# Performance work log

Hardware: AMD Instinct MI355X
Metric: run time of the kernel (lower is better)

Reference implementation:

```python
import jax, jax.numpy as jnp
import numpy as np

C_QKV = 128
C_HID = 32
N_HEADS = 4
INF = 1e9


def setup_inputs() -> dict:
    key = jax.random.key(0)
    ks = jax.random.split(key, 8)
    B, S = 256, 256
    hc = N_HEADS * C_HID  # 128
    inp = {
        "input_qkv": jax.random.normal(ks[0], (1, B, S, C_QKV), dtype=jnp.float32),
        "mask": jnp.ones((1, B, 1, 1, S), dtype=jnp.float32),
        "bias": jax.random.normal(ks[1], (1, 1, N_HEADS, S, S), dtype=jnp.float32),
        "add_transposed_output_to": jax.random.normal(ks[2], (1, B, S, C_QKV), dtype=jnp.float32),
        # linear_qkvg: Linear(c_qkv, 4*h*c), bias=False -> weight [4*hc, c_qkv]
        "W_qkvg": jax.random.normal(ks[3], (4 * hc, C_QKV), dtype=jnp.float32) * (1.0 / np.sqrt(C_QKV)),
        # gating bias initialized to ones in the module
        "linear_g_bias": jnp.ones((hc,), dtype=jnp.float32),
        # linear_o: Linear(hc, c_qkv), init='final' (zeros in AF2, use small random for a nontrivial test)
        "W_o": jax.random.normal(ks[4], (C_QKV, hc), dtype=jnp.float32) * (1.0 / np.sqrt(hc)),
        "b_o": jax.random.normal(ks[5], (C_QKV,), dtype=jnp.float32) * 0.02,
    }
    return inp


def reference(input_qkv, mask, bias, add_transposed_output_to, W_qkvg, linear_g_bias, W_o, b_o):
    hc = N_HEADS * C_HID
    # fused QKVG projection: [1, b, s, 4*hc]
    qkvg = jnp.einsum("xbsc,fc->xbsf", input_qkv, W_qkvg)
    q, k, v, g = jnp.split(qkvg, 4, axis=-1)
    # reshape to heads: [1, b, s, h, c]
    shp = q.shape[:-1] + (N_HEADS, C_HID)
    q = q.reshape(shp)
    k = k.reshape(shp)
    v = v.reshape(shp)
    scale = 1.0 / np.sqrt(C_HID)
    # scores: [1, b, h, q, k]
    a = jnp.einsum("xbqhc,xbkhc->xbhqk", q * scale, k)
    a = a + (mask - 1.0) * INF + bias
    a = jax.nn.softmax(a, axis=-1)
    # attention output: [1, b, q, h, c] -> [1, b, s, hc]
    o = jnp.einsum("xbhqk,xbkhc->xbqhc", a, v)
    o = o.reshape(o.shape[:-2] + (hc,))
    # sigmoid gating
    o = o * jax.nn.sigmoid(g + linear_g_bias)
    # fused linear + transpose(-2,-3) + add
    proj = jnp.einsum("xbsf,of->xbso", o, W_o) + b_o  # [1, b, s, c_qkv]
    out = add_transposed_output_to + jnp.swapaxes(proj, -2, -3)  # [1, s, b, c_qkv]
    return out
```

## Files before the change

kernel.cpp:

```cpp
#include <hip/hip_runtime.h>
#include <math.h>

#define BB 256
#define SS 256
#define NH 4

typedef __attribute__((ext_vector_type(8))) short bfrag;
typedef __attribute__((ext_vector_type(4))) float ffrag;

__device__ inline unsigned short f2bf(float x) {
    unsigned u = __float_as_uint(x);
    u += 0x7FFF + ((u >> 16) & 1);
    return (unsigned short)(u >> 16);
}
__device__ inline float bf2f(unsigned short h) {
    return __uint_as_float(((unsigned)h) << 16);
}
__device__ inline unsigned pack2(float a, float b) {
    return (unsigned)f2bf(a) | ((unsigned)f2bf(b) << 16);
}
union FragU { unsigned u[4]; bfrag b; };

#define XB_OFF  0
#define WB_OFF  8388608
#define WOB_OFF 8454144
#define OG_OFF  8470528

__global__ __launch_bounds__(256) void k0_cast(
    const float* __restrict__ X, const float* __restrict__ W,
    const float* __restrict__ Wo, unsigned short* __restrict__ dst)
{
    const int gid = blockIdx.x * 256 + threadIdx.x;
    const int XN8 = 8388608 / 8, WN8 = 65536 / 8, WoN8 = 16384 / 8;
    const float* src;
    size_t soff, doff;
    if (gid < XN8)            { src = X;  soff = (size_t)gid * 8;                 doff = XB_OFF + soff; }
    else if (gid < XN8 + WN8) { src = W;  soff = (size_t)(gid - XN8) * 8;         doff = WB_OFF + soff; }
    else if (gid < XN8 + WN8 + WoN8) { src = Wo; soff = (size_t)(gid - XN8 - WN8) * 8; doff = WOB_OFF + soff; }
    else return;
    const float4 a = *(const float4*)(src + soff);
    const float4 b = *(const float4*)(src + soff + 4);
    unsigned r0 = pack2(a.x, a.y), r1 = pack2(a.z, a.w);
    unsigned r2 = pack2(b.x, b.y), r3 = pack2(b.z, b.w);
    uint4 o; o.x = r0; o.y = r1; o.z = r2; o.w = r3;
    *(uint4*)(dst + doff) = o;
}

__global__ __launch_bounds__(256, 2) void k_fused(
    const unsigned short* __restrict__ Xb,
    const unsigned short* __restrict__ Wb,
    const float* __restrict__ gbias,
    const float* __restrict__ mask,
    const float* __restrict__ bias,
    unsigned short* __restrict__ og)
{
    const int h = blockIdx.x, b = blockIdx.y;
    const int t = threadIdx.x;
    const int w = t >> 6, lane = t & 63, l15 = lane & 15, quad = lane >> 4;

    __shared__ unsigned short Qb[SS * 40];
    __shared__ unsigned short Kb[SS * 40];
    __shared__ unsigned short Vt[32 * 264];
    __shared__ unsigned short Gb[SS * 34];
    __shared__ float maskLds[SS];

    maskLds[t] = (mask[b * SS + t] - 1.0f) * 1e9f;

    const float qscale = 0.17677669529663687f;

    for (int half = 0; half < 2; ++half) {
        bfrag Wfr[4][4];
#pragma unroll
        for (int f4 = 0; f4 < 4; ++f4) {
            const int floc = (half * 4 + f4) * 16 + l15;
            const int grow = (floc >> 5) * 128 + h * 32 + (floc & 31);
#pragma unroll
            for (int cc = 0; cc < 4; ++cc)
                Wfr[f4][cc] = *(const bfrag*)(Wb + grow * 128 + cc * 32 + quad * 8);
        }
#pragma unroll
        for (int st = 0; st < 4; ++st) {
            const int s = w * 64 + st * 16 + l15;
            bfrag Xfr[4];
#pragma unroll
            for (int cc = 0; cc < 4; ++cc)
                Xfr[cc] = *(const bfrag*)(Xb + (b * SS + s) * 128 + cc * 32 + quad * 8);
#pragma unroll
            for (int f4 = 0; f4 < 4; ++f4) {
                ffrag D = {0.f, 0.f, 0.f, 0.f};
#pragma unroll
                for (int cc = 0; cc < 4; ++cc)
                    D = __builtin_amdgcn_mfma_f32_16x16x32_bf16(Xfr[cc], Wfr[f4][cc], D, 0, 0, 0);
                const int ft = half * 4 + f4;
                const int fcol = ft * 16 + l15;
                const int srow0 = w * 64 + st * 16 + quad * 4;
                if (ft < 2) {
#pragma unroll
                    for (int r = 0; r < 4; ++r)
                        Qb[(srow0 + r) * 40 + fcol] = f2bf(D[r] * qscale);
                } else if (ft < 4) {
#pragma unroll
                    for (int r = 0; r < 4; ++r)
                        Kb[(srow0 + r) * 40 + (fcol - 32)] = f2bf(D[r]);
                } else if (ft < 6) {
                    const int base = (fcol - 64) * 264 + srow0;
                    *(unsigned*)&Vt[base]     = pack2(D[0], D[1]);
                    *(unsigned*)&Vt[base + 2] = pack2(D[2], D[3]);
                } else {
                    const int c = fcol - 96;
                    const float gb = gbias[h * 32 + c];
#pragma unroll
                    for (int r = 0; r < 4; ++r) {
                        const float g = 1.0f / (1.0f + __expf(-(D[r] + gb)));
                        Gb[(srow0 + r) * 34 + c] = f2bf(g);
                    }
                }
            }
        }
    }
    __syncthreads();

    bfrag Vfr[2][8];
#pragma unroll
    for (int ch = 0; ch < 2; ++ch)
#pragma unroll
        for (int ck = 0; ck < 8; ++ck)
            Vfr[ch][ck] = *(const bfrag*)&Vt[(ch * 16 + l15) * 264 + ck * 32 + quad * 8];

    const int srcA = l15 + ((quad & 1) * 2) * 16;
    const int srcB = srcA + 16;
    const bool hi = (quad >> 1) != 0;

    for (int qq = 0; qq < 4; ++qq) {
        const int q = w * 64 + qq * 16 + l15;
        const bfrag Qfr = *(const bfrag*)&Qb[q * 40 + quad * 8];

        ffrag S[16];
#pragma unroll
        for (int kt = 0; kt < 16; ++kt) {
            const bfrag Kfr = *(const bfrag*)&Kb[(kt * 16 + l15) * 40 + quad * 8];
            const ffrag z = {0.f, 0.f, 0.f, 0.f};
            S[kt] = __builtin_amdgcn_mfma_f32_16x16x32_bf16(Kfr, Qfr, z, 0, 0, 0);
        }

        const float* brow = bias + (h * SS + q) * SS;
        float m = -1e30f;
#pragma unroll
        for (int kt = 0; kt < 16; ++kt) {
            const float4 bv = *(const float4*)(brow + kt * 16 + quad * 4);
            const float4 mv = *(const float4*)(maskLds + kt * 16 + quad * 4);
            S[kt][0] += bv.x + mv.x; S[kt][1] += bv.y + mv.y;
            S[kt][2] += bv.z + mv.z; S[kt][3] += bv.w + mv.w;
            m = fmaxf(m, fmaxf(fmaxf(S[kt][0], S[kt][1]), fmaxf(S[kt][2], S[kt][3])));
        }
        m = fmaxf(m, __shfl_xor(m, 16, 64));
        m = fmaxf(m, __shfl_xor(m, 32, 64));

        float l = 0.f;
        unsigned pk[16][2];
#pragma unroll
        for (int kt = 0; kt < 16; ++kt) {
            const float p0 = __expf(S[kt][0] - m);
            const float p1 = __expf(S[kt][1] - m);
            const float p2 = __expf(S[kt][2] - m);
            const float p3 = __expf(S[kt][3] - m);
            l += (p0 + p1) + (p2 + p3);
            pk[kt][0] = pack2(p0, p1);
            pk[kt][1] = pack2(p2, p3);
        }
        l += __shfl_xor(l, 16, 64);
        l += __shfl_xor(l, 32, 64);

        ffrag O[2];
        O[0] = (ffrag){0.f, 0.f, 0.f, 0.f};
        O[1] = (ffrag){0.f, 0.f, 0.f, 0.f};
#pragma unroll
        for (int ck = 0; ck < 8; ++ck) {
            const unsigned a0 = (unsigned)__shfl((int)pk[2 * ck][0],     srcA, 64);
            const unsigned b0 = (unsigned)__shfl((int)pk[2 * ck + 1][0], srcA, 64);
            const unsigned a1 = (unsigned)__shfl((int)pk[2 * ck][1],     srcA, 64);
            const unsigned b1 = (unsigned)__shfl((int)pk[2 * ck + 1][1], srcA, 64);
            const unsigned a2 = (unsigned)__shfl((int)pk[2 * ck][0],     srcB, 64);
            const unsigned b2 = (unsigned)__shfl((int)pk[2 * ck + 1][0], srcB, 64);
            const unsigned a3 = (unsigned)__shfl((int)pk[2 * ck][1],     srcB, 64);
            const unsigned b3 = (unsigned)__shfl((int)pk[2 * ck + 1][1], srcB, 64);
            FragU fu;
            fu.u[0] = hi ? b0 : a0;
            fu.u[1] = hi ? b1 : a1;
            fu.u[2] = hi ? b2 : a2;
            fu.u[3] = hi ? b3 : a3;
            O[0] = __builtin_amdgcn_mfma_f32_16x16x32_bf16(Vfr[0][ck], fu.b, O[0], 0, 0, 0);
            O[1] = __builtin_amdgcn_mfma_f32_16x16x32_bf16(Vfr[1][ck], fu.b, O[1], 0, 0, 0);
        }

        const float invl = 1.0f / l;
        const unsigned short* gr = &Gb[q * 34];
        unsigned* orow = (unsigned*)(og + (b * SS + q) * 128 + h * 32);
#pragma unroll
        for (int ch = 0; ch < 2; ++ch) {
            const int c0 = ch * 16 + quad * 4;
            const float v0 = O[ch][0] * invl * bf2f(gr[c0 + 0]);
            const float v1 = O[ch][1] * invl * bf2f(gr[c0 + 1]);
            const float v2 = O[ch][2] * invl * bf2f(gr[c0 + 2]);
            const float v3 = O[ch][3] * invl * bf2f(gr[c0 + 3]);
            orow[(c0 >> 1) + 0] = pack2(v0, v1);
            orow[(c0 >> 1) + 1] = pack2(v2, v3);
        }
    }
}

__global__ __launch_bounds__(256) void k3_proj(
    const unsigned short* __restrict__ ogb,
    const unsigned short* __restrict__ Wob,
    const float* __restrict__ bo,
    const float* __restrict__ addt,
    float* __restrict__ out)
{
    const int j = blockIdx.x, ih = blockIdx.y;
    const int t = threadIdx.x;
    const int w = t >> 6, lane = t & 63, l15 = lane & 15, quad = lane >> 4;

    __shared__ unsigned short OgS[64 * 136];
    __shared__ float OutS[64 * 132];

    {
        const int ss = t >> 2;
        const int c32 = (t & 3) * 32;
        const unsigned short* src = ogb + (((size_t)j * SS + ih * 64 + ss) * 128) + c32;
        unsigned short* dst = &OgS[ss * 136 + c32];
#pragma unroll
        for (int u = 0; u < 4; ++u)
            *(uint4*)(dst + u * 8) = *(const uint4*)(src + u * 8);
    }

    bfrag Wfr[2][4];
#pragma unroll
    for (int ctl = 0; ctl < 2; ++ctl) {
        const int crow = (w * 2 + ctl) * 16 + l15;
#pragma unroll
        for (int cc = 0; cc < 4; ++cc)
            Wfr[ctl][cc] = *(const bfrag*)(Wob + crow * 128 + cc * 32 + quad * 8);
    }
    const float bo0 = bo[(w * 2 + 0) * 16 + l15];
    const float bo1 = bo[(w * 2 + 1) * 16 + l15];

    __syncthreads();

#pragma unroll
    for (int jt = 0; jt < 4; ++jt) {
        bfrag Ab[4];
#pragma unroll
        for (int cc = 0; cc < 4; ++cc)
            Ab[cc] = *(const bfrag*)&OgS[(jt * 16 + l15) * 136 + cc * 32 + quad * 8];

        ffrag D0 = {0.f, 0.f, 0.f, 0.f};
        ffrag D1 = {0.f, 0.f, 0.f, 0.f};
#pragma unroll
        for (int cc = 0; cc < 4; ++cc) {
            D0 = __builtin_amdgcn_mfma_f32_16x16x32_bf16(Ab[cc], Wfr[0][cc], D0, 0, 0, 0);
            D1 = __builtin_amdgcn_mfma_f32_16x16x32_bf16(Ab[cc], Wfr[1][cc], D1, 0, 0, 0);
        }

        const int c0 = (w * 2 + 0) * 16 + l15;
        const int c1 = (w * 2 + 1) * 16 + l15;
#pragma unroll
        for (int r = 0; r < 4; ++r) {
            const int row = jt * 16 + quad * 4 + r;
            OutS[row * 132 + c0] = D0[r] + bo0;
            OutS[row * 132 + c1] = D1[r] + bo1;
        }
    }
    __syncthreads();

    {
        const int c4 = lane & 31;
        const int rsub = t >> 5;
#pragma unroll
        for (int v = 0; v < 8; ++v) {
            const int row = v * 8 + rsub;
            const int s = ih * 64 + row;
            const size_t off = ((size_t)s * BB + j) * 128 + c4 * 4;
            const float4 av = *(const float4*)(addt + off);
            const float4 dv = *(const float4*)&OutS[row * 132 + c4 * 4];
            float4 ov;
            ov.x = dv.x + av.x; ov.y = dv.y + av.y;
            ov.z = dv.z + av.z; ov.w = dv.w + av.w;
            *(float4*)(out + off) = ov;
        }
    }
}

extern "C" void kernel_launch(void* const* d_in, const int* in_sizes, int n_in,
                              void* d_out, int out_size, void* d_ws, size_t ws_size,
                              hipStream_t stream) {
    const float* X     = (const float*)d_in[0];
    const float* mask  = (const float*)d_in[1];
    const float* bias  = (const float*)d_in[2];
    const float* addt  = (const float*)d_in[3];
    const float* Wqkvg = (const float*)d_in[4];
    const float* gbias = (const float*)d_in[5];
    const float* Wo    = (const float*)d_in[6];
    const float* bo    = (const float*)d_in[7];
    float* out = (float*)d_out;

    unsigned short* ws = (unsigned short*)d_ws;
    unsigned short* Xb  = ws + XB_OFF;
    unsigned short* Wb  = ws + WB_OFF;
    unsigned short* Wob = ws + WOB_OFF;
    unsigned short* og  = ws + OG_OFF;

    k0_cast<<<4136, 256, 0, stream>>>(X, Wqkvg, Wo, ws);
    k_fused<<<dim3(NH, BB), 256, 0, stream>>>(Xb, Wb, gbias, mask, bias, og);
    k3_proj<<<dim3(BB, 4), 256, 0, stream>>>(og, Wob, bo, addt, out);
}
```

Baseline: 232.8 us.

## Keep Q and gate fragments in registers instead of LDS, raise occupancy

Result: slower. 359.0 us (+54.2%).

```diff
diff --git a/kernel.cpp b/kernel.cpp
--- a/kernel.cpp
+++ b/kernel.cpp
@@ -46,7 +46,7 @@
     *(uint4*)(dst + doff) = o;
 }
 
-__global__ __launch_bounds__(256, 2) void k_fused(
+__global__ __launch_bounds__(256, 3) void k_fused(
     const unsigned short* __restrict__ Xb,
     const unsigned short* __restrict__ Wb,
     const float* __restrict__ gbias,
@@ -58,16 +58,21 @@
     const int t = threadIdx.x;
     const int w = t >> 6, lane = t & 63, l15 = lane & 15, quad = lane >> 4;
 
-    __shared__ unsigned short Qb[SS * 40];
     __shared__ unsigned short Kb[SS * 40];
     __shared__ unsigned short Vt[32 * 264];
-    __shared__ unsigned short Gb[SS * 34];
     __shared__ float maskLds[SS];
 
     maskLds[t] = (mask[b * SS + t] - 1.0f) * 1e9f;
 
     const float qscale = 0.17677669529663687f;
 
+    FragU qa0, qa1, qa2, qa3;
+    unsigned g0c0a, g0c0b, g0c1a, g0c1b;
+    unsigned g1c0a, g1c0b, g1c1a, g1c1b;
+    unsigned g2c0a, g2c0b, g2c1a, g2c1b;
+    unsigned g3c0a, g3c0b, g3c1a, g3c1b;
+
+#pragma unroll
     for (int half = 0; half < 2; ++half) {
         bfrag Wfr[4][4];
 #pragma unroll
@@ -87,33 +92,56 @@
                 Xfr[cc] = *(const bfrag*)(Xb + (b * SS + s) * 128 + cc * 32 + quad * 8);
 #pragma unroll
             for (int f4 = 0; f4 < 4; ++f4) {
-                ffrag D = {0.f, 0.f, 0.f, 0.f};
-#pragma unroll
-                for (int cc = 0; cc < 4; ++cc)
-                    D = __builtin_amdgcn_mfma_f32_16x16x32_bf16(Xfr[cc], Wfr[f4][cc], D, 0, 0, 0);
                 const int ft = half * 4 + f4;
-                const int fcol = ft * 16 + l15;
-                const int srow0 = w * 64 + st * 16 + quad * 4;
                 if (ft < 2) {
+                    ffrag D = {0.f, 0.f, 0.f, 0.f};
+#pragma unroll
+                    for (int cc = 0; cc < 4; ++cc)
+                        D = __builtin_amdgcn_mfma_f32_16x16x32_bf16(Wfr[f4][cc], Xfr[cc], D, 0, 0, 0);
+                    const unsigned lo = pack2(D[0] * qscale, D[1] * qscale);
+                    const unsigned hi = pack2(D[2] * qscale, D[3] * qscale);
+                    FragU* qa = (st == 0) ? &qa0 : (st == 1) ? &qa1 : (st == 2) ? &qa2 : &qa3;
+                    if (ft == 0) { qa->u[0] = lo; qa->u[1] = hi; }
+                    else         { qa->u[2] = lo; qa->u[3] = hi; }
+                } else if (ft < 4) {
+                    ffrag D = {0.f, 0.f, 0.f, 0.f};
+#pragma unroll
+                    for (int cc = 0; cc < 4; ++cc)
+                        D = __builtin_amdgcn_mfma_f32_16x16x32_bf16(Xfr[cc], Wfr[f4][cc], D, 0, 0, 0);
+                    const int c = (ft - 2) * 16 + l15;
+                    const int p = ((c & 15) >> 2) * 8 + (c & 3) + ((c >> 4) << 2);
+                    const int srow0 = w * 64 + st * 16 + quad * 4;
 #pragma unroll
                     for (int r = 0; r < 4; ++r)
-                        Qb[(srow0 + r) * 40 + fcol] = f2bf(D[r] * qscale);
-                } else if (ft < 4) {
-#pragma unroll
-                    for (int r = 0; r < 4; ++r)
-                        Kb[(srow0 + r) * 40 + (fcol - 32)] = f2bf(D[r]);
+                        Kb[(srow0 + r) * 40 + p] = f2bf(D[r]);
                 } else if (ft < 6) {
+                    ffrag D = {0.f, 0.f, 0.f, 0.f};
+#pragma unroll
+                    for (int cc = 0; cc < 4; ++cc)
+                        D = __builtin_amdgcn_mfma_f32_16x16x32_bf16(Xfr[cc], Wfr[f4][cc], D, 0, 0, 0);
+                    const int fcol = ft * 16 + l15;
+                    const int srow0 = w * 64 + st * 16 + quad * 4;
                     const int base = (fcol - 64) * 264 + srow0;
                     *(unsigned*)&Vt[base]     = pack2(D[0], D[1]);
                     *(unsigned*)&Vt[base + 2] = pack2(D[2], D[3]);
                 } else {
-                    const int c = fcol - 96;
-                    const float gb = gbias[h * 32 + c];
+                    ffrag D = {0.f, 0.f, 0.f, 0.f};
+#pragma unroll
+                    for (int cc = 0; cc < 4; ++cc)
+                        D = __builtin_amdgcn_mfma_f32_16x16x32_bf16(Wfr[f4][cc], Xfr[cc], D, 0, 0, 0);
+                    const int ch = ft - 6;
+                    float gv[4];
 #pragma unroll
                     for (int r = 0; r < 4; ++r) {
-                        const float g = 1.0f / (1.0f + __expf(-(D[r] + gb)));
-                        Gb[(srow0 + r) * 34 + c] = f2bf(g);
+                        const float gb = gbias[h * 32 + ch * 16 + quad * 4 + r];
+                        gv[r] = 1.0f / (1.0f + __expf(-(D[r] + gb)));
                     }
+                    const unsigned pa = pack2(gv[0], gv[1]);
+                    const unsigned pb = pack2(gv[2], gv[3]);
+                    if (st == 0) { if (ch == 0) { g0c0a = pa; g0c0b = pb; } else { g0c1a = pa; g0c1b = pb; } }
+                    if (st == 1) { if (ch == 0) { g1c0a = pa; g1c0b = pb; } else { g1c1a = pa; g1c1b = pb; } }
+                    if (st == 2) { if (ch == 0) { g2c0a = pa; g2c0b = pb; } else { g2c1a = pa; g2c1b = pb; } }
+                    if (st == 3) { if (ch == 0) { g3c0a = pa; g3c0b = pb; } else { g3c1a = pa; g3c1b = pb; } }
                 }
             }
         }
@@ -133,7 +161,12 @@
 
     for (int qq = 0; qq < 4; ++qq) {
         const int q = w * 64 + qq * 16 + l15;
-        const bfrag Qfr = *(const bfrag*)&Qb[q * 40 + quad * 8];
+        bfrag Qfr;
+        unsigned gc0a, gc0b, gc1a, gc1b;
+        if (qq == 0)      { Qfr = qa0.b; gc0a = g0c0a; gc0b = g0c0b; gc1a = g0c1a; gc1b = g0c1b; }
+        else if (qq == 1) { Qfr = qa1.b; gc0a = g1c0a; gc0b = g1c0b; gc1a = g1c1a; gc1b = g1c1b; }
+        else if (qq == 2) { Qfr = qa2.b; gc0a = g2c0a; gc0b = g2c0b; gc1a = g2c1a; gc1b = g2c1b; }
+        else              { Qfr = qa3.b; gc0a = g3c0a; gc0b = g3c0b; gc1a = g3c1a; gc1b = g3c1b; }
 
         ffrag S[16];
 #pragma unroll
@@ -194,15 +227,16 @@
         }
 
         const float invl = 1.0f / l;
-        const unsigned short* gr = &Gb[q * 34];
         unsigned* orow = (unsigned*)(og + (b * SS + q) * 128 + h * 32);
 #pragma unroll
         for (int ch = 0; ch < 2; ++ch) {
+            const unsigned ga = ch ? gc1a : gc0a;
+            const unsigned gb2 = ch ? gc1b : gc0b;
             const int c0 = ch * 16 + quad * 4;
-            const float v0 = O[ch][0] * invl * bf2f(gr[c0 + 0]);
-            const float v1 = O[ch][1] * invl * bf2f(gr[c0 + 1]);
-            const float v2 = O[ch][2] * invl * bf2f(gr[c0 + 2]);
-            const float v3 = O[ch][3] * invl * bf2f(gr[c0 + 3]);
+            const float v0 = O[ch][0] * invl * bf2f((unsigned short)(ga & 0xffff));
+            const float v1 = O[ch][1] * invl * bf2f((unsigned short)(ga >> 16));
+            const float v2 = O[ch][2] * invl * bf2f((unsigned short)(gb2 & 0xffff));
+            const float v3 = O[ch][3] * invl * bf2f((unsigned short)(gb2 >> 16));
             orow[(c0 >> 1) + 0] = pack2(v0, v1);
             orow[(c0 >> 1) + 1] = pack2(v2, v3);
         }
```
